# Optimization experiments

Measured on AMD Instinct MI355X. Metric: run time of the kernel, lower is better.

Reference implementation:

```python
import jax, jax.numpy as jnp
import numpy as np

BIN_SIZE = 500      # bin_size from __init__
K = 5               # num_neighbors
DIST_MULT = 0.1
MAX_NUM_BINS = 200


def setup_inputs() -> dict:
    key = jax.random.key(0)
    k1, k2 = jax.random.split(key)
    points = jax.random.normal(k1, (2, 5000, 64), dtype=jnp.float32)
    # codebook_random_rotations: [n_features, max_num_bins // 2]
    rotations = jax.random.normal(k2, (64, MAX_NUM_BINS // 2), dtype=jnp.float32)
    return {"points": points, "rotations": rotations}


def reference(points, rotations):
    """Dense equivalent of the batched tf.SparseTensor output [B, N, N].

    tf.sparse.add sums duplicate (src, dst) entries, which scatter-add
    reproduces exactly.
    """
    B, N, F = points.shape
    nbins = N // BIN_SIZE

    # LSH projection: use first nbins//2 rotation columns, mirror with -mul.
    mul = jnp.einsum('bnf,fh->bnh', points, rotations[:, : nbins // 2])
    cmul = jnp.concatenate([mul, -mul], axis=-1)          # [B, N, nbins]
    bin_idx = jnp.argmax(cmul, axis=-1)                   # [B, N]
    # split_indices_to_bins: stable argsort of bin assignment, reshape to bins
    bins_split = jnp.argsort(bin_idx, axis=-1, stable=True).reshape(B, nbins, BIN_SIZE)

    # gather points into bins: [B, nbins, BIN_SIZE, F]
    parts = jnp.take_along_axis(points, bins_split.reshape(B, N, 1), axis=1)
    parts = parts.reshape(B, nbins, BIN_SIZE, F)

    # pairwise_dist within each bin
    na = jnp.sum(parts * parts, axis=-1)                  # [B, nbins, bs]
    gram = jnp.einsum('bgif,bgjf->bgij', parts, parts)    # [B, nbins, bs, bs]
    dm = jnp.sqrt(jnp.maximum(na[..., :, None] - 2.0 * gram + na[..., None, :], 1e-6))
    aff = jnp.exp(-DIST_MULT * dm)                        # [B, nbins, bs, bs]

    # top-k neighbors per point within its bin
    vals, idx = jax.lax.top_k(aff, K)                     # [B, nbins, bs, K]

    # map local bin indices back to global point indices
    dst = jax.vmap(jax.vmap(lambda b, i: b[i]))(bins_split, idx)   # [B, nbins, bs, K]
    src = jnp.broadcast_to(bins_split[..., None], dst.shape)
    b_ix = jnp.broadcast_to(jnp.arange(B)[:, None, None, None], dst.shape)

    # scatter-add (duplicates summed, as in repeated tf.sparse.add)
    out = jnp.zeros((B, N, N), dtype=points.dtype)
    out = out.at[b_ix, src, dst].add(vals)
    return out
```

## Files before the change

kernel.cpp:

```cpp
#include <hip/hip_runtime.h>
#include <cfloat>
#include <cstddef>

#define NBATCH 2
#define NPTS   5000
#define NF     64
#define NB     10
#define BINSZ  500
#define TOPK   5
#define ROTCOLS 100
#define ROW4   (NPTS / 4)

__global__ __launch_bounds__(256) void bin_norm_k(const float* __restrict__ pts,
                                                  const float* __restrict__ rot,
                                                  int* __restrict__ bin_idx,
                                                  float* __restrict__ na) {
    __shared__ float srot[NF * 5];
    const int t = threadIdx.x;
    for (int i = t; i < NF * 5; i += 256) {
        int f = i / 5, h = i - 5 * f;
        srot[i] = rot[f * ROTCOLS + h];
    }
    __syncthreads();

    int pt   = blockIdx.x * 4 + (t >> 6);
    int lane = t & 63;
    float p  = pts[(size_t)pt * NF + lane];
    float nn = p * p;
    float c0 = p * srot[lane * 5 + 0];
    float c1 = p * srot[lane * 5 + 1];
    float c2 = p * srot[lane * 5 + 2];
    float c3 = p * srot[lane * 5 + 3];
    float c4 = p * srot[lane * 5 + 4];
    #pragma unroll
    for (int off = 32; off > 0; off >>= 1) {
        nn += __shfl_xor(nn, off);
        c0 += __shfl_xor(c0, off);
        c1 += __shfl_xor(c1, off);
        c2 += __shfl_xor(c2, off);
        c3 += __shfl_xor(c3, off);
        c4 += __shfl_xor(c4, off);
    }
    if (lane == 0) {
        float c[5] = {c0, c1, c2, c3, c4};
        float bv = c[0]; int bi = 0;
        #pragma unroll
        for (int h = 1; h < 5; ++h) if (c[h] > bv) { bv = c[h]; bi = h; }
        #pragma unroll
        for (int h = 0; h < 5; ++h) if (-c[h] > bv) { bv = -c[h]; bi = h + 5; }
        bin_idx[pt] = bi;
        na[pt] = nn;
    }
}

__global__ __launch_bounds__(256) void sort_k(const int* __restrict__ bin_idx,
                                              int* __restrict__ order) {
    const int b = blockIdx.x;
    const int t = threadIdx.x;
    const int w = t >> 6, lane = t & 63;
    __shared__ int sh_bin[NPTS];
    __shared__ int sh_hist[256][NB];
    __shared__ int sh_part[NB][16];
    __shared__ int sh_tot[NB + 1];

    for (int i = t; i < NPTS; i += 256) sh_bin[i] = bin_idx[b * NPTS + i];
    #pragma unroll
    for (int h = 0; h < NB; ++h) sh_hist[t][h] = 0;
    __syncthreads();

    const int CH = (NPTS + 255) / 256;
    const int i0 = t * CH;
    const int i1 = (i0 + CH < NPTS) ? (i0 + CH) : NPTS;
    for (int i = i0; i < i1; ++i) sh_hist[t][sh_bin[i]]++;
    __syncthreads();

    if (t < NB * 16) {
        int h = t >> 4, s = t & 15;
        int sum = 0;
        #pragma unroll
        for (int k = 0; k < 16; ++k) sum += sh_hist[s * 16 + k][h];
        sh_part[h][s] = sum;
    }
    __syncthreads();
    if (t < NB) {
        int tot = 0;
        #pragma unroll
        for (int s = 0; s < 16; ++s) tot += sh_part[t][s];
        sh_tot[t + 1] = tot;
    }
    __syncthreads();
    if (t == 0) {
        sh_tot[0] = 0;
        for (int h = 1; h <= NB; ++h) sh_tot[h] += sh_tot[h - 1];
    }
    __syncthreads();

    for (int h = w; h < NB; h += 4) {
        int base = lane * 4;
        int v0 = sh_hist[base + 0][h];
        int v1 = sh_hist[base + 1][h];
        int v2 = sh_hist[base + 2][h];
        int v3 = sh_hist[base + 3][h];
        int lt = v0 + v1 + v2 + v3;
        int x = lt;
        #pragma unroll
        for (int off = 1; off < 64; off <<= 1) {
            int y = __shfl_up(x, off);
            if (lane >= off) x += y;
        }
        int excl = x - lt + sh_tot[h];
        sh_hist[base + 0][h] = excl;
        sh_hist[base + 1][h] = excl + v0;
        sh_hist[base + 2][h] = excl + v0 + v1;
        sh_hist[base + 3][h] = excl + v0 + v1 + v2;
    }
    __syncthreads();

    for (int i = i0; i < i1; ++i) {
        int h = sh_bin[i];
        order[b * NPTS + sh_hist[t][h]++] = i;
    }
}

__global__ __launch_bounds__(256) void pair_topk_k(const float* __restrict__ pts,
                                                   const float* __restrict__ na,
                                                   const int* __restrict__ order,
                                                   float* __restrict__ wv,
                                                   int* __restrict__ wd) {
    const int bx  = blockIdx.x;
    const int g   = bx >> 3;
    const int rb  = bx & 7;
    const int b   = g / NB;
    const int grp = g % NB;
    const int r0  = rb * 64;
    const int tid = threadIdx.x;
    const int w   = tid >> 6;
    const int lane = tid & 63;

    __shared__ float sh_pts[BINSZ * NF];
    __shared__ float sh_na[BINSZ];
    __shared__ int   sh_idx[BINSZ];
    __shared__ float sh_mv[4][64][TOPK];
    __shared__ int   sh_mi[4][64][TOPK];

    const int* ord = order + b * NPTS + grp * BINSZ;
    for (int i = tid; i < BINSZ; i += 256) sh_idx[i] = ord[i];
    __syncthreads();

    const float* pbase = pts + (size_t)b * NPTS * NF;
    float4* sp4 = (float4*)sh_pts;
    for (int q = tid; q < BINSZ * (NF / 4); q += 256) {
        int j = q >> 4, f4 = q & 15;
        sp4[q] = ((const float4*)(pbase + (size_t)sh_idx[j] * NF))[f4];
    }
    for (int i = tid; i < BINSZ; i += 256) sh_na[i] = na[b * NPTS + sh_idx[i]];
    __syncthreads();

    const int rr  = r0 + lane;
    const int rcl = (rr < BINSZ) ? rr : (BINSZ - 1);
    float4 rowr[16];
    #pragma unroll
    for (int q = 0; q < 16; ++q) rowr[q] = sp4[rcl * 16 + q];
    const float na_r = sh_na[rcl];

    float tv[TOPK]; int ti[TOPK];
    #pragma unroll
    for (int s = 0; s < TOPK; ++s) { tv[s] = FLT_MAX; ti[s] = 0; }

    const int cbase = w * 125;
    for (int jj = 0; jj < 125; ++jj) {
        const int j = cbase + jj;
        const float4* cp = sp4 + j * 16;
        float acc = 0.f;
        #pragma unroll
        for (int q = 0; q < 16; ++q) {
            float4 cc = cp[q];
            acc += rowr[q].x * cc.x;
            acc += rowr[q].y * cc.y;
            acc += rowr[q].z * cc.z;
            acc += rowr[q].w * cc.w;
        }
        float d2 = na_r - 2.f * acc + sh_na[j];
        if (d2 < tv[TOPK - 1]) {
            tv[TOPK - 1] = d2; ti[TOPK - 1] = j;
            #pragma unroll
            for (int s = TOPK - 1; s > 0; --s) {
                if (tv[s] < tv[s - 1]) {
                    float fv = tv[s]; tv[s] = tv[s - 1]; tv[s - 1] = fv;
                    int   fi = ti[s]; ti[s] = ti[s - 1]; ti[s - 1] = fi;
                }
            }
        }
    }

    #pragma unroll
    for (int s = 0; s < TOPK; ++s) { sh_mv[w][lane][s] = tv[s]; sh_mi[w][lane][s] = ti[s]; }
    __syncthreads();

    if (tid < 64) {
        const int r = tid;
        if (r0 + r < BINSZ) {
            int h0 = 0, h1 = 0, h2 = 0, h3 = 0;
            const int src = sh_idx[r0 + r];
            const size_t gbase = ((size_t)b * NPTS + src) * TOPK;
            #pragma unroll
            for (int s = 0; s < TOPK; ++s) {
                float v0 = sh_mv[0][r][h0];
                float v1 = sh_mv[1][r][h1];
                float v2 = sh_mv[2][r][h2];
                float v3 = sh_mv[3][r][h3];
                float best = v0; int bw = 0;
                if (v1 < best) { best = v1; bw = 1; }
                if (v2 < best) { best = v2; bw = 2; }
                if (v3 < best) { best = v3; bw = 3; }
                int j;
                if      (bw == 0) { j = sh_mi[0][r][h0]; h0++; }
                else if (bw == 1) { j = sh_mi[1][r][h1]; h1++; }
                else if (bw == 2) { j = sh_mi[2][r][h2]; h2++; }
                else              { j = sh_mi[3][r][h3]; h3++; }
                float dm  = sqrtf(fmaxf(best, 1e-6f));
                wv[gbase + s] = expf(-0.1f * dm);
                wd[gbase + s] = sh_idx[j];
            }
        }
    }
}

__global__ __launch_bounds__(256) void zero_inject_k(const float* __restrict__ wv,
                                                     const int* __restrict__ wd,
                                                     float* __restrict__ out) {
    const int t = threadIdx.x;
    const size_t gr0 = (size_t)blockIdx.x * 4;
    float4* o4 = ((float4*)out) + gr0 * ROW4;
    const float4 z4 = make_float4(0.f, 0.f, 0.f, 0.f);
    for (int i = t; i < 4 * ROW4; i += 256) o4[i] = z4;
    __syncthreads();
    if (t < 4 * TOPK) {
        int r = t / TOPK, s = t - r * TOPK;
        size_t g = gr0 + r;
        out[g * NPTS + wd[g * TOPK + s]] = wv[g * TOPK + s];
    }
}

extern "C" void kernel_launch(void* const* d_in, const int* in_sizes, int n_in,
                              void* d_out, int out_size, void* d_ws, size_t ws_size,
                              hipStream_t stream) {
    const float* points = (const float*)d_in[0];
    const float* rot    = (const float*)d_in[1];
    float* out = (float*)d_out;

    char* ws = (char*)d_ws;
    int*   bin_idx = (int*)ws;                                   ws += NBATCH * NPTS * sizeof(int);
    float* na      = (float*)ws;                                 ws += NBATCH * NPTS * sizeof(float);
    int*   order   = (int*)ws;                                   ws += NBATCH * NPTS * sizeof(int);
    float* wv      = (float*)ws;                                 ws += NBATCH * NPTS * TOPK * sizeof(float);
    int*   wd      = (int*)ws;

    bin_norm_k<<<(NBATCH * NPTS) / 4, 256, 0, stream>>>(points, rot, bin_idx, na);
    sort_k<<<NBATCH, 256, 0, stream>>>(bin_idx, order);
    pair_topk_k<<<NBATCH * NB * 8, 256, 0, stream>>>(points, na, order, wv, wd);
    zero_inject_k<<<(NBATCH * NPTS) / 4, 256, 0, stream>>>(wv, wd, out);
}
```

Measured before the change: 114.2 us.

## Overlap output zeroing with pairwise top-k and split columns across blocks

The output zero-fill moves into the pairwise kernel as extra blocks, so the 200MB memset runs concurrently with the distance/top-k compute blocks. Compute is now split by column chunks of 64: each block stages only 64 columns in shared memory, and each thread handles two rows over those columns, writing partial top-5 lists per chunk. A new merge kernel selects the final top-5 from the 40 candidates and scatters them after zeroing is complete. The cost is more workspace traffic and one extra merge pass over the candidate lists.

Measured after the change: 92.02 us. -19.4%, faster.

```diff
diff --git a/kernel.cpp b/kernel.cpp
--- a/kernel.cpp
+++ b/kernel.cpp
@@ -9,7 +9,13 @@
 #define BINSZ  500
 #define TOPK   5
 #define ROTCOLS 100
-#define ROW4   (NPTS / 4)
+
+#define NCB    8
+#define CBS    64
+#define NCAND  (NCB * TOPK)
+#define NCOMP  (NBATCH * NB * NCB)
+#define NZERO  1888
+#define OUT4   (NBATCH * NPTS * NPTS / 4)
 
 __global__ __launch_bounds__(256) void bin_norm_k(const float* __restrict__ pts,
                                                   const float* __restrict__ rot,
@@ -122,123 +128,146 @@
     }
 }
 
-__global__ __launch_bounds__(256) void pair_topk_k(const float* __restrict__ pts,
+__global__ __launch_bounds__(256) void pair_zero_k(const float* __restrict__ pts,
                                                    const float* __restrict__ na,
                                                    const int* __restrict__ order,
                                                    float* __restrict__ wv,
-                                                   int* __restrict__ wd) {
+                                                   int* __restrict__ wd,
+                                                   float* __restrict__ out) {
     const int bx  = blockIdx.x;
-    const int g   = bx >> 3;
-    const int rb  = bx & 7;
+    const int tid = threadIdx.x;
+
+    if (bx >= NCOMP) {
+        const int z = bx - NCOMP;
+        const int chunk = (OUT4 + NZERO - 1) / NZERO;
+        const size_t base = (size_t)z * chunk;
+        size_t end = base + chunk; if (end > (size_t)OUT4) end = OUT4;
+        float4* o4 = (float4*)out;
+        const float4 z4 = make_float4(0.f, 0.f, 0.f, 0.f);
+        for (size_t i = base + tid; i < end; i += 256) o4[i] = z4;
+        return;
+    }
+
+    const int g   = bx / NCB;
+    const int cb  = bx - g * NCB;
     const int b   = g / NB;
-    const int grp = g % NB;
-    const int r0  = rb * 64;
-    const int tid = threadIdx.x;
-    const int w   = tid >> 6;
-    const int lane = tid & 63;
-
-    __shared__ float sh_pts[BINSZ * NF];
-    __shared__ float sh_na[BINSZ];
-    __shared__ int   sh_idx[BINSZ];
-    __shared__ float sh_mv[4][64][TOPK];
-    __shared__ int   sh_mi[4][64][TOPK];
+    const int grp = g - b * NB;
+    const int c0  = cb * CBS;
+    const int ncols = (c0 + CBS <= BINSZ) ? CBS : (BINSZ - c0);
+
+    __shared__ float sh_cols[CBS * NF];
+    __shared__ float sh_cna[CBS];
 
     const int* ord = order + b * NPTS + grp * BINSZ;
-    for (int i = tid; i < BINSZ; i += 256) sh_idx[i] = ord[i];
-    __syncthreads();
-
-    const float* pbase = pts + (size_t)b * NPTS * NF;
-    float4* sp4 = (float4*)sh_pts;
-    for (int q = tid; q < BINSZ * (NF / 4); q += 256) {
-        int j = q >> 4, f4 = q & 15;
-        sp4[q] = ((const float4*)(pbase + (size_t)sh_idx[j] * NF))[f4];
-    }
-    for (int i = tid; i < BINSZ; i += 256) sh_na[i] = na[b * NPTS + sh_idx[i]];
-    __syncthreads();
-
-    const int rr  = r0 + lane;
-    const int rcl = (rr < BINSZ) ? rr : (BINSZ - 1);
-    float4 rowr[16];
-    #pragma unroll
-    for (int q = 0; q < 16; ++q) rowr[q] = sp4[rcl * 16 + q];
-    const float na_r = sh_na[rcl];
-
-    float tv[TOPK]; int ti[TOPK];
-    #pragma unroll
-    for (int s = 0; s < TOPK; ++s) { tv[s] = FLT_MAX; ti[s] = 0; }
-
-    const int cbase = w * 125;
-    for (int jj = 0; jj < 125; ++jj) {
-        const int j = cbase + jj;
-        const float4* cp = sp4 + j * 16;
-        float acc = 0.f;
+    const float4* p4 = (const float4*)(pts + (size_t)b * NPTS * NF);
+    float4* sc4 = (float4*)sh_cols;
+
+    for (int i = tid; i < ncols * 16; i += 256) {
+        int c = i >> 4, q = i & 15;
+        sc4[c * 16 + q] = p4[(size_t)ord[c0 + c] * 16 + q];
+    }
+    if (tid < ncols) sh_cna[tid] = na[b * NPTS + ord[c0 + tid]];
+    __syncthreads();
+
+    const int p0 = tid, p1 = tid + 256;
+    const bool h1 = (p1 < BINSZ);
+    const int gi0 = ord[p0];
+    const int gi1 = h1 ? ord[p1] : gi0;
+    float4 r0[16], r1[16];
+    #pragma unroll
+    for (int q = 0; q < 16; ++q) {
+        r0[q] = p4[(size_t)gi0 * 16 + q];
+        r1[q] = p4[(size_t)gi1 * 16 + q];
+    }
+    const float na0 = na[b * NPTS + gi0];
+    const float na1 = na[b * NPTS + gi1];
+
+    float tv0[TOPK], tv1[TOPK]; int tp0[TOPK], tp1[TOPK];
+    #pragma unroll
+    for (int s = 0; s < TOPK; ++s) { tv0[s] = FLT_MAX; tv1[s] = FLT_MAX; tp0[s] = 0; tp1[s] = 0; }
+
+    for (int c = 0; c < ncols; ++c) {
+        const float4* cq = sc4 + c * 16;
+        float a0 = 0.f, a1 = 0.f;
         #pragma unroll
         for (int q = 0; q < 16; ++q) {
-            float4 cc = cp[q];
-            acc += rowr[q].x * cc.x;
-            acc += rowr[q].y * cc.y;
-            acc += rowr[q].z * cc.z;
-            acc += rowr[q].w * cc.w;
-        }
-        float d2 = na_r - 2.f * acc + sh_na[j];
-        if (d2 < tv[TOPK - 1]) {
-            tv[TOPK - 1] = d2; ti[TOPK - 1] = j;
+            float4 cc = cq[q];
+            a0 += r0[q].x * cc.x; a0 += r0[q].y * cc.y;
+            a0 += r0[q].z * cc.z; a0 += r0[q].w * cc.w;
+            a1 += r1[q].x * cc.x; a1 += r1[q].y * cc.y;
+            a1 += r1[q].z * cc.z; a1 += r1[q].w * cc.w;
+        }
+        const float cna = sh_cna[c];
+        const int pos = c0 + c;
+        float d0 = na0 - 2.f * a0 + cna;
+        float d1 = na1 - 2.f * a1 + cna;
+        if (d0 < tv0[TOPK - 1]) {
+            tv0[TOPK - 1] = d0; tp0[TOPK - 1] = pos;
             #pragma unroll
             for (int s = TOPK - 1; s > 0; --s) {
-                if (tv[s] < tv[s - 1]) {
-                    float fv = tv[s]; tv[s] = tv[s - 1]; tv[s - 1] = fv;
-                    int   fi = ti[s]; ti[s] = ti[s - 1]; ti[s - 1] = fi;
+                if (tv0[s] < tv0[s - 1]) {
+                    float fv = tv0[s]; tv0[s] = tv0[s - 1]; tv0[s - 1] = fv;
+                    int   fi = tp0[s]; tp0[s] = tp0[s - 1]; tp0[s - 1] = fi;
                 }
             }
         }
-    }
-
-    #pragma unroll
-    for (int s = 0; s < TOPK; ++s) { sh_mv[w][lane][s] = tv[s]; sh_mi[w][lane][s] = ti[s]; }
-    __syncthreads();
-
-    if (tid < 64) {
-        const int r = tid;
-        if (r0 + r < BINSZ) {
-            int h0 = 0, h1 = 0, h2 = 0, h3 = 0;
-            const int src = sh_idx[r0 + r];
-            const size_t gbase = ((size_t)b * NPTS + src) * TOPK;
+        if (h1 && d1 < tv1[TOPK - 1]) {
+            tv1[TOPK - 1] = d1; tp1[TOPK - 1] = pos;
             #pragma unroll
-            for (int s = 0; s < TOPK; ++s) {
-                float v0 = sh_mv[0][r][h0];
-                float v1 = sh_mv[1][r][h1];
-                float v2 = sh_mv[2][r][h2];
-                float v3 = sh_mv[3][r][h3];
-                float best = v0; int bw = 0;
-                if (v1 < best) { best = v1; bw = 1; }
-                if (v2 < best) { best = v2; bw = 2; }
-                if (v3 < best) { best = v3; bw = 3; }
-                int j;
-                if      (bw == 0) { j = sh_mi[0][r][h0]; h0++; }
-                else if (bw == 1) { j = sh_mi[1][r][h1]; h1++; }
-                else if (bw == 2) { j = sh_mi[2][r][h2]; h2++; }
-                else              { j = sh_mi[3][r][h3]; h3++; }
-                float dm  = sqrtf(fmaxf(best, 1e-6f));
-                wv[gbase + s] = expf(-0.1f * dm);
-                wd[gbase + s] = sh_idx[j];
+            for (int s = TOPK - 1; s > 0; --s) {
+                if (tv1[s] < tv1[s - 1]) {
+                    float fv = tv1[s]; tv1[s] = tv1[s - 1]; tv1[s - 1] = fv;
+                    int   fi = tp1[s]; tp1[s] = tp1[s - 1]; tp1[s - 1] = fi;
+                }
             }
         }
     }
-}
-
-__global__ __launch_bounds__(256) void zero_inject_k(const float* __restrict__ wv,
-                                                     const int* __restrict__ wd,
-                                                     float* __restrict__ out) {
-    const int t = threadIdx.x;
-    const size_t gr0 = (size_t)blockIdx.x * 4;
-    float4* o4 = ((float4*)out) + gr0 * ROW4;
-    const float4 z4 = make_float4(0.f, 0.f, 0.f, 0.f);
-    for (int i = t; i < 4 * ROW4; i += 256) o4[i] = z4;
-    __syncthreads();
-    if (t < 4 * TOPK) {
-        int r = t / TOPK, s = t - r * TOPK;
-        size_t g = gr0 + r;
-        out[g * NPTS + wd[g * TOPK + s]] = wv[g * TOPK + s];
+
+    const int slotbase = (b * NB + grp) * BINSZ;
+    {
+        size_t wbase = ((size_t)(slotbase + p0) * NCB + cb) * TOPK;
+        #pragma unroll
+        for (int s = 0; s < TOPK; ++s) { wv[wbase + s] = tv0[s]; wd[wbase + s] = tp0[s]; }
+    }
+    if (h1) {
+        size_t wbase = ((size_t)(slotbase + p1) * NCB + cb) * TOPK;
+        #pragma unroll
+        for (int s = 0; s < TOPK; ++s) { wv[wbase + s] = tv1[s]; wd[wbase + s] = tp1[s]; }
+    }
+}
+
+__global__ __launch_bounds__(256) void merge_inject_k(const float* __restrict__ wv,
+                                                      const int* __restrict__ wd,
+                                                      const int* __restrict__ order,
+                                                      float* __restrict__ out) {
+    const int slot = blockIdx.x * 256 + threadIdx.x;
+    if (slot >= NBATCH * NPTS) return;
+    const int b   = slot / (NB * BINSZ);
+    const int rem = slot - b * NB * BINSZ;
+    const int grp = rem / BINSZ;
+    const int p   = rem - grp * BINSZ;
+    const int* ord = order + b * NPTS + grp * BINSZ;
+    const int src = ord[p];
+
+    float cv[NCAND]; int cp[NCAND];
+    const size_t base = (size_t)slot * NCAND;
+    #pragma unroll
+    for (int k = 0; k < NCAND; ++k) { cv[k] = wv[base + k]; cp[k] = wd[base + k]; }
+
+    unsigned long long used = 0;
+    float* orow = out + ((size_t)b * NPTS + src) * NPTS;
+    #pragma unroll
+    for (int s = 0; s < TOPK; ++s) {
+        float bv = FLT_MAX; int bp = 0x7fffffff; int bk = 0;
+        #pragma unroll
+        for (int k = 0; k < NCAND; ++k) {
+            bool ok = !((used >> k) & 1ull);
+            bool better = ok && ((cv[k] < bv) || (cv[k] == bv && cp[k] < bp));
+            if (better) { bv = cv[k]; bp = cp[k]; bk = k; }
+        }
+        used |= (1ull << bk);
+        float val = expf(-0.1f * sqrtf(fmaxf(bv, 1e-6f)));
+        orow[ord[bp]] = val;
     }
 }
 
@@ -250,14 +279,14 @@
     float* out = (float*)d_out;
 
     char* ws = (char*)d_ws;
-    int*   bin_idx = (int*)ws;                                   ws += NBATCH * NPTS * sizeof(int);
-    float* na      = (float*)ws;                                 ws += NBATCH * NPTS * sizeof(float);
-    int*   order   = (int*)ws;                                   ws += NBATCH * NPTS * sizeof(int);
-    float* wv      = (float*)ws;                                 ws += NBATCH * NPTS * TOPK * sizeof(float);
+    int*   bin_idx = (int*)ws;   ws += NBATCH * NPTS * sizeof(int);
+    float* na      = (float*)ws; ws += NBATCH * NPTS * sizeof(float);
+    int*   order   = (int*)ws;   ws += NBATCH * NPTS * sizeof(int);
+    float* wv      = (float*)ws; ws += (size_t)NBATCH * NPTS * NCAND * sizeof(float);
     int*   wd      = (int*)ws;
 
     bin_norm_k<<<(NBATCH * NPTS) / 4, 256, 0, stream>>>(points, rot, bin_idx, na);
     sort_k<<<NBATCH, 256, 0, stream>>>(bin_idx, order);
-    pair_topk_k<<<NBATCH * NB * 8, 256, 0, stream>>>(points, na, order, wv, wd);
-    zero_inject_k<<<(NBATCH * NPTS) / 4, 256, 0, stream>>>(wv, wd, out);
-}
+    pair_zero_k<<<NCOMP + NZERO, 256, 0, stream>>>(points, na, order, wv, wd, out);
+    merge_inject_k<<<(NBATCH * NPTS + 255) / 256, 256, 0, stream>>>(wv, wd, order, out);
+}
```

## Fuse output zeroing into binning kernel and inject top-k directly from pair kernel

Applied to the files above, without the earlier changes.

Zeroing of the 200MB dense output moves into extra blocks of the first (binning) kernel, so it runs early and overlaps with the LSH projection work. The separate zero+inject kernel and its workspace buffers go away; the pair kernel now writes the top-k values straight into the output. The pair kernel also drops its shared-memory staging of the bin. Each wave loads column points from global memory and broadcasts them with readlane, and there are 8 waves per block instead of 4, which changes occupancy and the load pattern. The risk is higher global/L2 traffic for column fetches and the cost of a serial readlane loop.

New measurement: 104.4 us. 1.09x faster.

```diff
diff --git a/kernel.cpp b/kernel.cpp
--- a/kernel.cpp
+++ b/kernel.cpp
@@ -9,14 +9,28 @@
 #define BINSZ  500
 #define TOPK   5
 #define ROTCOLS 100
-#define ROW4   (NPTS / 4)
-
-__global__ __launch_bounds__(256) void bin_norm_k(const float* __restrict__ pts,
-                                                  const float* __restrict__ rot,
-                                                  int* __restrict__ bin_idx,
-                                                  float* __restrict__ na) {
+
+#define NZ     3500
+#define OUT4   (NBATCH * NPTS * NPTS / 4)
+#define CPW    63
+
+__global__ __launch_bounds__(256) void bin_norm_zero_k(const float* __restrict__ pts,
+                                                       const float* __restrict__ rot,
+                                                       int* __restrict__ bin_idx,
+                                                       float* __restrict__ na,
+                                                       float* __restrict__ out) {
+    const int t = threadIdx.x;
+    if (blockIdx.x >= 2500) {
+        const int z = blockIdx.x - 2500;
+        const int chunk = (OUT4 + NZ - 1) / NZ;
+        const size_t base = (size_t)z * chunk;
+        size_t end = base + chunk; if (end > (size_t)OUT4) end = OUT4;
+        float4* o4 = (float4*)out;
+        const float4 z4 = make_float4(0.f, 0.f, 0.f, 0.f);
+        for (size_t i = base + t; i < end; i += 256) o4[i] = z4;
+        return;
+    }
     __shared__ float srot[NF * 5];
-    const int t = threadIdx.x;
     for (int i = t; i < NF * 5; i += 256) {
         int f = i / 5, h = i - 5 * f;
         srot[i] = rot[f * ROTCOLS + h];
@@ -122,123 +136,90 @@
     }
 }
 
-__global__ __launch_bounds__(256) void pair_topk_k(const float* __restrict__ pts,
-                                                   const float* __restrict__ na,
-                                                   const int* __restrict__ order,
-                                                   float* __restrict__ wv,
-                                                   int* __restrict__ wd) {
-    const int bx  = blockIdx.x;
-    const int g   = bx >> 3;
-    const int rb  = bx & 7;
-    const int b   = g / NB;
-    const int grp = g % NB;
-    const int r0  = rb * 64;
-    const int tid = threadIdx.x;
-    const int w   = tid >> 6;
+__global__ __launch_bounds__(512) void pair_merge_inject_k(const float* __restrict__ pts,
+                                                           const float* __restrict__ na,
+                                                           const int* __restrict__ order,
+                                                           float* __restrict__ out) {
+    const int bx   = blockIdx.x;
+    const int g    = bx >> 3;
+    const int rb   = bx & 7;
+    const int b    = g / NB;
+    const int grp  = g - b * NB;
+    const int tid  = threadIdx.x;
+    const int w    = tid >> 6;
     const int lane = tid & 63;
 
-    __shared__ float sh_pts[BINSZ * NF];
-    __shared__ float sh_na[BINSZ];
-    __shared__ int   sh_idx[BINSZ];
-    __shared__ float sh_mv[4][64][TOPK];
-    __shared__ int   sh_mi[4][64][TOPK];
+    __shared__ float sh_mv[8][64][TOPK];
+    __shared__ int   sh_mi[8][64][TOPK];
 
     const int* ord = order + b * NPTS + grp * BINSZ;
-    for (int i = tid; i < BINSZ; i += 256) sh_idx[i] = ord[i];
-    __syncthreads();
-
-    const float* pbase = pts + (size_t)b * NPTS * NF;
-    float4* sp4 = (float4*)sh_pts;
-    for (int q = tid; q < BINSZ * (NF / 4); q += 256) {
-        int j = q >> 4, f4 = q & 15;
-        sp4[q] = ((const float4*)(pbase + (size_t)sh_idx[j] * NF))[f4];
-    }
-    for (int i = tid; i < BINSZ; i += 256) sh_na[i] = na[b * NPTS + sh_idx[i]];
-    __syncthreads();
-
-    const int rr  = r0 + lane;
-    const int rcl = (rr < BINSZ) ? rr : (BINSZ - 1);
-    float4 rowr[16];
-    #pragma unroll
-    for (int q = 0; q < 16; ++q) rowr[q] = sp4[rcl * 16 + q];
-    const float na_r = sh_na[rcl];
-
-    float tv[TOPK]; int ti[TOPK];
-    #pragma unroll
-    for (int s = 0; s < TOPK; ++s) { tv[s] = FLT_MAX; ti[s] = 0; }
-
-    const int cbase = w * 125;
-    for (int jj = 0; jj < 125; ++jj) {
-        const int j = cbase + jj;
-        const float4* cp = sp4 + j * 16;
+    const float*  pb  = pts + (size_t)b * NPTS * NF;
+    const float4* p4  = (const float4*)pb;
+    const float*  nab = na + b * NPTS;
+
+    const int prow = rb * 64 + lane;
+    const int pcl  = (prow < BINSZ) ? prow : (BINSZ - 1);
+    const int gi   = ord[pcl];
+    float4 r[16];
+    #pragma unroll
+    for (int q = 0; q < 16; ++q) r[q] = p4[(size_t)gi * 16 + q];
+    const float* rf = (const float*)r;
+    const float na_r = nab[gi];
+
+    float tv[TOPK]; int tp[TOPK];
+    #pragma unroll
+    for (int s = 0; s < TOPK; ++s) { tv[s] = FLT_MAX; tp[s] = 0; }
+
+    const int c_lo = w * CPW;
+    const int c_hi = (c_lo + CPW < BINSZ) ? (c_lo + CPW) : BINSZ;
+    for (int cj = c_lo; cj < c_hi; ++cj) {
+        const int gc = ord[cj];
+        const float colv = pb[(size_t)gc * NF + lane];
+        const float cna  = nab[gc];
         float acc = 0.f;
         #pragma unroll
-        for (int q = 0; q < 16; ++q) {
-            float4 cc = cp[q];
-            acc += rowr[q].x * cc.x;
-            acc += rowr[q].y * cc.y;
-            acc += rowr[q].z * cc.z;
-            acc += rowr[q].w * cc.w;
-        }
-        float d2 = na_r - 2.f * acc + sh_na[j];
+        for (int k = 0; k < 64; ++k) {
+            float bc = __uint_as_float(__builtin_amdgcn_readlane(__float_as_uint(colv), k));
+            acc += rf[k] * bc;
+        }
+        float d2 = na_r - 2.f * acc + cna;
         if (d2 < tv[TOPK - 1]) {
-            tv[TOPK - 1] = d2; ti[TOPK - 1] = j;
+            tv[TOPK - 1] = d2; tp[TOPK - 1] = cj;
             #pragma unroll
             for (int s = TOPK - 1; s > 0; --s) {
                 if (tv[s] < tv[s - 1]) {
                     float fv = tv[s]; tv[s] = tv[s - 1]; tv[s - 1] = fv;
-                    int   fi = ti[s]; ti[s] = ti[s - 1]; ti[s - 1] = fi;
+                    int   fi = tp[s]; tp[s] = tp[s - 1]; tp[s - 1] = fi;
                 }
             }
         }
     }
 
     #pragma unroll
-    for (int s = 0; s < TOPK; ++s) { sh_mv[w][lane][s] = tv[s]; sh_mi[w][lane][s] = ti[s]; }
+    for (int s = 0; s < TOPK; ++s) { sh_mv[w][lane][s] = tv[s]; sh_mi[w][lane][s] = tp[s]; }
     __syncthreads();
 
     if (tid < 64) {
-        const int r = tid;
-        if (r0 + r < BINSZ) {
-            int h0 = 0, h1 = 0, h2 = 0, h3 = 0;
-            const int src = sh_idx[r0 + r];
-            const size_t gbase = ((size_t)b * NPTS + src) * TOPK;
+        const int r_ = tid;
+        const int my = rb * 64 + r_;
+        if (my < BINSZ) {
+            int h[8] = {0, 0, 0, 0, 0, 0, 0, 0};
+            const int src = ord[my];
+            float* orow = out + ((size_t)b * NPTS + src) * NPTS;
             #pragma unroll
             for (int s = 0; s < TOPK; ++s) {
-                float v0 = sh_mv[0][r][h0];
-                float v1 = sh_mv[1][r][h1];
-                float v2 = sh_mv[2][r][h2];
-                float v3 = sh_mv[3][r][h3];
-                float best = v0; int bw = 0;
-                if (v1 < best) { best = v1; bw = 1; }
-                if (v2 < best) { best = v2; bw = 2; }
-                if (v3 < best) { best = v3; bw = 3; }
-                int j;
-                if      (bw == 0) { j = sh_mi[0][r][h0]; h0++; }
-                else if (bw == 1) { j = sh_mi[1][r][h1]; h1++; }
-                else if (bw == 2) { j = sh_mi[2][r][h2]; h2++; }
-                else              { j = sh_mi[3][r][h3]; h3++; }
-                float dm  = sqrtf(fmaxf(best, 1e-6f));
-                wv[gbase + s] = expf(-0.1f * dm);
-                wd[gbase + s] = sh_idx[j];
+                float best = sh_mv[0][r_][h[0]]; int bw = 0;
+                #pragma unroll
+                for (int ww = 1; ww < 8; ++ww) {
+                    float v = sh_mv[ww][r_][h[ww]];
+                    if (v < best) { best = v; bw = ww; }
+                }
+                const int j = sh_mi[bw][r_][h[bw]];
+                h[bw]++;
+                float val = expf(-0.1f * sqrtf(fmaxf(best, 1e-6f)));
+                orow[ord[j]] = val;
             }
         }
-    }
-}
-
-__global__ __launch_bounds__(256) void zero_inject_k(const float* __restrict__ wv,
-                                                     const int* __restrict__ wd,
-                                                     float* __restrict__ out) {
-    const int t = threadIdx.x;
-    const size_t gr0 = (size_t)blockIdx.x * 4;
-    float4* o4 = ((float4*)out) + gr0 * ROW4;
-    const float4 z4 = make_float4(0.f, 0.f, 0.f, 0.f);
-    for (int i = t; i < 4 * ROW4; i += 256) o4[i] = z4;
-    __syncthreads();
-    if (t < 4 * TOPK) {
-        int r = t / TOPK, s = t - r * TOPK;
-        size_t g = gr0 + r;
-        out[g * NPTS + wd[g * TOPK + s]] = wv[g * TOPK + s];
     }
 }
 
@@ -250,14 +231,11 @@
     float* out = (float*)d_out;
 
     char* ws = (char*)d_ws;
-    int*   bin_idx = (int*)ws;                                   ws += NBATCH * NPTS * sizeof(int);
-    float* na      = (float*)ws;                                 ws += NBATCH * NPTS * sizeof(float);
-    int*   order   = (int*)ws;                                   ws += NBATCH * NPTS * sizeof(int);
-    float* wv      = (float*)ws;                                 ws += NBATCH * NPTS * TOPK * sizeof(float);
-    int*   wd      = (int*)ws;
-
-    bin_norm_k<<<(NBATCH * NPTS) / 4, 256, 0, stream>>>(points, rot, bin_idx, na);
+    int*   bin_idx = (int*)ws;   ws += NBATCH * NPTS * sizeof(int);
+    float* na      = (float*)ws; ws += NBATCH * NPTS * sizeof(float);
+    int*   order   = (int*)ws;
+
+    bin_norm_zero_k<<<2500 + NZ, 256, 0, stream>>>(points, rot, bin_idx, na, out);
     sort_k<<<NBATCH, 256, 0, stream>>>(bin_idx, order);
-    pair_topk_k<<<NBATCH * NB * 8, 256, 0, stream>>>(points, na, order, wv, wd);
-    zero_inject_k<<<(NBATCH * NPTS) / 4, 256, 0, stream>>>(wv, wd, out);
-}
+    pair_merge_inject_k<<<NBATCH * NB * 8, 512, 0, stream>>>(points, na, order, out);
+}
```
